# Kernel tuning notes

Hardware: AMD Instinct MI355X
Metric: run time of the kernel (lower is better)

Reference implementation:

```python
import jax, jax.numpy as jnp
import numpy as np

LEVELS = [(128, 128), (64, 64), (32, 32), (16, 16)]  # (H_l, W_l) per feature level
N_TOTAL = sum(h * w for h, w in LEVELS)  # 21760
B, D, H, P, L = 2, 256, 8, 4, 4
HD = D // H
FFN_DIM = 1024


def setup_inputs() -> dict:
    key = jax.random.key(0)
    ks = jax.random.split(key, 12)
    s = 0.02  # weight init scale
    return {
        'embed': jax.random.normal(ks[0], (B, N_TOTAL, D), jnp.float32),
        'pos': jax.random.normal(ks[1], (B, N_TOTAL, D), jnp.float32),
        'ref_points': jax.random.uniform(ks[2], (B, N_TOTAL, L, 2), jnp.float32),
        'ln1_w': jnp.ones((D,), jnp.float32), 'ln1_b': jnp.zeros((D,), jnp.float32),
        'ln2_w': jnp.ones((D,), jnp.float32), 'ln2_b': jnp.zeros((D,), jnp.float32),
        'Wv': jax.random.normal(ks[3], (D, D), jnp.float32) * s, 'bv': jnp.zeros((D,), jnp.float32),
        'Woff': jax.random.normal(ks[4], (D, H * L * P * 2), jnp.float32) * s, 'boff': jnp.zeros((H * L * P * 2,), jnp.float32),
        'Wattn': jax.random.normal(ks[5], (D, H * L * P), jnp.float32) * s, 'battn': jnp.zeros((H * L * P,), jnp.float32),
        'Wo': jax.random.normal(ks[6], (D, D), jnp.float32) * s, 'bo': jnp.zeros((D,), jnp.float32),
        'W1': jax.random.normal(ks[7], (D, FFN_DIM), jnp.float32) * s, 'b1': jnp.zeros((FFN_DIM,), jnp.float32),
        'W2': jax.random.normal(ks[8], (FFN_DIM, D), jnp.float32) * s, 'b2': jnp.zeros((D,), jnp.float32),
        'dimensions': jnp.array(LEVELS, jnp.int32),
    }


def _layer_norm(x, w, b):
    m = jnp.mean(x, axis=-1, keepdims=True)
    v = jnp.mean(jnp.square(x - m), axis=-1, keepdims=True)
    return (x - m) * jax.lax.rsqrt(v + 1e-5) * w + b


def _msda(q, ref, v, dims, Wv, bv, Woff, boff, Wattn, battn, Wo, bo):
    # q, v: (B, N, D); ref: (B, N, L, 2) normalized (x, y)
    Bq, N, _ = q.shape
    value = (v @ Wv + bv).reshape(Bq, N, H, HD)
    off = (q @ Woff + boff).reshape(Bq, N, H, L, P, 2)
    aw = jax.nn.softmax((q @ Wattn + battn).reshape(Bq, N, H, L * P), axis=-1)
    aw = aw.reshape(Bq, N, H, L, P)
    # offset normalizer is [W_l, H_l]
    norm = jnp.stack([dims[:, 1], dims[:, 0]], axis=-1).astype(q.dtype)  # (L, 2)
    loc = ref[:, :, None, :, None, :] + off / norm[None, None, None, :, None, :]  # (B,N,H,L,P,2)

    out = jnp.zeros((Bq, N, H, HD), q.dtype)
    start = 0
    for l, (Hl, Wl) in enumerate(LEVELS):
        S = Hl * Wl
        vl = value[:, start:start + S].transpose(0, 2, 1, 3)  # (B, H, S, hd)
        start += S
        # grid_sample semantics: align_corners=False, zero padding
        x = loc[:, :, :, l, :, 0] * Wl - 0.5  # (B, N, H, P)
        y = loc[:, :, :, l, :, 1] * Hl - 0.5
        x0 = jnp.floor(x); y0 = jnp.floor(y)
        wx = x - x0; wy = y - y0
        x0i = x0.astype(jnp.int32); y0i = y0.astype(jnp.int32)
        samp = jnp.zeros(x.shape + (HD,), q.dtype)
        for dy, dx, w in ((0, 0, (1 - wx) * (1 - wy)), (0, 1, wx * (1 - wy)),
                          (1, 0, (1 - wx) * wy), (1, 1, wx * wy)):
            xi = x0i + dx; yi = y0i + dy
            valid = (xi >= 0) & (xi < Wl) & (yi >= 0) & (yi < Hl)
            idx = jnp.clip(yi, 0, Hl - 1) * Wl + jnp.clip(xi, 0, Wl - 1)  # (B, N, H, P)
            idx_t = idx.transpose(0, 2, 1, 3).reshape(Bq, H, N * P)
            g = jnp.take_along_axis(vl, idx_t[..., None], axis=2)  # (B, H, N*P, hd)
            g = g.reshape(Bq, H, N, P, HD).transpose(0, 2, 1, 3, 4)  # (B, N, H, P, hd)
            samp = samp + (w * valid)[..., None] * g
        out = out + jnp.sum(samp * aw[:, :, :, l, :, None], axis=3)
    return out.reshape(Bq, N, D) @ Wo + bo


def reference(embed, pos, ref_points, ln1_w, ln1_b, ln2_w, ln2_b, Wv, bv, Woff, boff,
              Wattn, battn, Wo, bo, W1, b1, W2, b2, dimensions):
    v = _layer_norm(embed, ln1_w, ln1_b)
    q = v + pos
    embed = embed + _msda(q, ref_points, v, dimensions, Wv, bv, Woff, boff, Wattn, battn, Wo, bo)
    f = _layer_norm(embed, ln2_w, ln2_b)
    embed = embed + jax.nn.relu(f @ W1 + b1) @ W2 + b2
    return embed
```

## Files before the change

### kernel.cpp

```cpp
#include <hip/hip_runtime.h>
#include <cstdint>
#include <cstddef>

#define N_TOTAL 21760
#define BATCH   2
#define M_TOT   (BATCH * N_TOTAL)
#define DMODEL  256
#define NHEAD   8
#define HDIM    32
#define FFN     1024

typedef __bf16 b16x8 __attribute__((ext_vector_type(8)));
typedef float  f32x4 __attribute__((ext_vector_type(4)));

typedef const __attribute__((address_space(1))) void g_void;
typedef __attribute__((address_space(3))) void lds_void;

__device__ __forceinline__ unsigned short f2b(float f) {
  union { float f; unsigned u; } v; v.f = f;
  unsigned r = v.u + 0x7FFF + ((v.u >> 16) & 1);
  return (unsigned short)(r >> 16);
}
__device__ __forceinline__ float b2f(unsigned short u) {
  union { unsigned u; float f; } v; v.u = (unsigned)u << 16;
  return v.f;
}

__global__ void wconv_all(const float* __restrict__ Wv, const float* __restrict__ Woff,
                          const float* __restrict__ Wattn, const float* __restrict__ Wo,
                          const float* __restrict__ W1, const float* __restrict__ W2,
                          unsigned short* __restrict__ dstbase) {
  int idx = blockIdx.x * 256 + threadIdx.x;
  const float* src; int K, N, off;
  if (idx < 65536)       { src = Wv;    K = 256;  N = 256;  off = 0;      }
  else if (idx < 131072) { src = Woff;  K = 256;  N = 256;  off = 65536;  idx -= 65536; }
  else if (idx < 163840) { src = Wattn; K = 256;  N = 128;  off = 131072; idx -= 131072; }
  else if (idx < 229376) { src = Wo;    K = 256;  N = 256;  off = 163840; idx -= 163840; }
  else if (idx < 491520) { src = W1;    K = 256;  N = 1024; off = 229376; idx -= 229376; }
  else if (idx < 753664) { src = W2;    K = 1024; N = 256;  off = 491520; idx -= 491520; }
  else return;
  int k = idx / N, n = idx - k * N;
  dstbase[off + (size_t)n * K + k] = f2b(src[idx]);
}

__global__ void ln1_kernel(const float* __restrict__ x, const float* __restrict__ pos,
                           const float* __restrict__ w, const float* __restrict__ b,
                           unsigned short* __restrict__ vb, unsigned short* __restrict__ qb) {
  int t = threadIdx.x;
  int tkn = blockIdx.x * 4 + (t >> 6);
  int lane = t & 63;
  size_t base = (size_t)tkn * DMODEL + lane * 4;
  float4 xv = *(const float4*)&x[base];
  float s1 = xv.x + xv.y + xv.z + xv.w;
  float s2 = xv.x * xv.x + xv.y * xv.y + xv.z * xv.z + xv.w * xv.w;
  #pragma unroll
  for (int off = 32; off; off >>= 1) {
    s1 += __shfl_down(s1, off);
    s2 += __shfl_down(s2, off);
  }
  s1 = __shfl(s1, 0); s2 = __shfl(s2, 0);
  float m   = s1 * (1.0f / DMODEL);
  float var = s2 * (1.0f / DMODEL) - m * m;
  float rs  = rsqrtf(var + 1e-5f);
  float4 wv = *(const float4*)&w[lane * 4];
  float4 bv = *(const float4*)&b[lane * 4];
  float4 pv = *(const float4*)&pos[base];
  float o0 = (xv.x - m) * rs * wv.x + bv.x;
  float o1 = (xv.y - m) * rs * wv.y + bv.y;
  float o2 = (xv.z - m) * rs * wv.z + bv.z;
  float o3 = (xv.w - m) * rs * wv.w + bv.w;
  ushort4 vo = {f2b(o0), f2b(o1), f2b(o2), f2b(o3)};
  ushort4 qo = {f2b(o0 + pv.x), f2b(o1 + pv.y), f2b(o2 + pv.z), f2b(o3 + pv.w)};
  *(ushort4*)&vb[base] = vo;
  *(ushort4*)&qb[base] = qo;
}

__global__ void ln2_kernel(const unsigned short* __restrict__ x, const float* __restrict__ w,
                           const float* __restrict__ b, unsigned short* __restrict__ yb) {
  int t = threadIdx.x;
  int tkn = blockIdx.x * 4 + (t >> 6);
  int lane = t & 63;
  size_t base = (size_t)tkn * DMODEL + lane * 4;
  ushort4 xu = *(const ushort4*)&x[base];
  float x0 = b2f(xu.x), x1 = b2f(xu.y), x2 = b2f(xu.z), x3 = b2f(xu.w);
  float s1 = x0 + x1 + x2 + x3;
  float s2 = x0 * x0 + x1 * x1 + x2 * x2 + x3 * x3;
  #pragma unroll
  for (int off = 32; off; off >>= 1) {
    s1 += __shfl_down(s1, off);
    s2 += __shfl_down(s2, off);
  }
  s1 = __shfl(s1, 0); s2 = __shfl(s2, 0);
  float m   = s1 * (1.0f / DMODEL);
  float var = s2 * (1.0f / DMODEL) - m * m;
  float rs  = rsqrtf(var + 1e-5f);
  float4 wv = *(const float4*)&w[lane * 4];
  float4 bv = *(const float4*)&b[lane * 4];
  ushort4 vo = {f2b((x0 - m) * rs * wv.x + bv.x), f2b((x1 - m) * rs * wv.y + bv.y),
                f2b((x2 - m) * rs * wv.z + bv.z), f2b((x3 - m) * rs * wv.w + bv.w)};
  *(ushort4*)&yb[base] = vo;
}

__device__ __forceinline__ void gemm_core(
    const unsigned short* __restrict__ A, const unsigned short* __restrict__ Bt,
    const float* __restrict__ bias,
    const float* __restrict__ addf, const unsigned short* __restrict__ addb,
    float* __restrict__ Cf, unsigned short* __restrict__ Cb,
    int K, int N, int relu, int row0, int col0,
    unsigned short* As, unsigned short* Bs) {
  int t  = threadIdx.x;
  int w  = t >> 6;
  int l  = t & 63;
  int wm = w >> 1, wn = w & 1;
  int lr = l & 15;
  int kq = l >> 4;

  f32x4 acc[4][4];
  #pragma unroll
  for (int i = 0; i < 4; ++i)
    #pragma unroll
    for (int j = 0; j < 4; ++j) acc[i][j] = (f32x4){0.f, 0.f, 0.f, 0.f};

  int srow = (l >> 3);
  int sseg = (l & 7) * 8;

  for (int k0 = 0; k0 < K; k0 += 64) {
    #pragma unroll
    for (int i = 0; i < 4; ++i) {
      int c = w * 4 + i;
      const unsigned short* ga = A  + (size_t)(row0 + c * 8 + srow) * K + k0 + sseg;
      const unsigned short* gb = Bt + (size_t)(col0 + c * 8 + srow) * K + k0 + sseg;
      __builtin_amdgcn_global_load_lds((g_void*)ga, (lds_void*)(As + c * 512), 16, 0, 0);
      __builtin_amdgcn_global_load_lds((g_void*)gb, (lds_void*)(Bs + c * 512), 16, 0, 0);
    }
    __syncthreads();
    #pragma unroll
    for (int kk = 0; kk < 2; ++kk) {
      b16x8 aF[4], bF[4];
      #pragma unroll
      for (int i = 0; i < 4; ++i)
        aF[i] = *(const b16x8*)&As[(wm * 64 + i * 16 + lr) * 64 + kk * 32 + kq * 8];
      #pragma unroll
      for (int j = 0; j < 4; ++j)
        bF[j] = *(const b16x8*)&Bs[(wn * 64 + j * 16 + lr) * 64 + kk * 32 + kq * 8];
      #pragma unroll
      for (int i = 0; i < 4; ++i)
        #pragma unroll
        for (int j = 0; j < 4; ++j)
          acc[i][j] = __builtin_amdgcn_mfma_f32_16x16x32_bf16(aF[i], bF[j], acc[i][j], 0, 0, 0);
    }
    __syncthreads();
  }

  #pragma unroll
  for (int j = 0; j < 4; ++j) {
    int colg = col0 + wn * 64 + j * 16 + lr;
    float bcol = bias[colg];
    #pragma unroll
    for (int i = 0; i < 4; ++i) {
      int r0g = row0 + wm * 64 + i * 16 + kq * 4;
      #pragma unroll
      for (int r = 0; r < 4; ++r) {
        int rowg = r0g + r;
        float o = acc[i][j][r] + bcol;
        if (relu) o = fmaxf(o, 0.0f);
        if (addf) o += addf[(size_t)rowg * N + colg];
        if (addb) o += b2f(addb[(size_t)rowg * N + colg]);
        if (Cf) Cf[(size_t)rowg * N + colg] = o;
        if (Cb) Cb[(size_t)rowg * N + colg] = f2b(o);
      }
    }
  }
}

__global__ __launch_bounds__(256, 3)
void gemm_bf16(const unsigned short* __restrict__ A,
               const unsigned short* __restrict__ Bt,
               const float* __restrict__ bias,
               const float* __restrict__ addf, const unsigned short* __restrict__ addb,
               float* __restrict__ Cf, unsigned short* __restrict__ Cb,
               int K, int N, int relu) {
  __shared__ unsigned short As[128 * 64];
  __shared__ unsigned short Bs[128 * 64];
  gemm_core(A, Bt, bias, addf, addb, Cf, Cb, K, N, relu,
            blockIdx.x * 128, blockIdx.y * 128, As, Bs);
}

__global__ __launch_bounds__(256, 3)
void gemm_proj(const unsigned short* __restrict__ vb,
               const unsigned short* __restrict__ qb,
               const unsigned short* __restrict__ Wvt,
               const unsigned short* __restrict__ Wofft,
               const unsigned short* __restrict__ Wattnt,
               const float* __restrict__ bv, const float* __restrict__ boff,
               const float* __restrict__ battn,
               unsigned short* __restrict__ valb,
               unsigned short* __restrict__ offb,
               unsigned short* __restrict__ awb) {
  __shared__ unsigned short As[128 * 64];
  __shared__ unsigned short Bs[128 * 64];
  int y = blockIdx.y;
  const unsigned short* A; const unsigned short* Bt; const float* bias;
  unsigned short* C; int col0, N;
  if (y < 2)      { A = vb; Bt = Wvt;    bias = bv;    C = valb; col0 = y * 128;       N = 256; }
  else if (y < 4) { A = qb; Bt = Wofft;  bias = boff;  C = offb; col0 = (y - 2) * 128; N = 256; }
  else            { A = qb; Bt = Wattnt; bias = battn; C = awb;  col0 = 0;             N = 128; }
  gemm_core(A, Bt, bias, nullptr, nullptr, nullptr, C, 256, N, 0,
            blockIdx.x * 128, col0, As, Bs);
}

__global__ void msda_kernel(const unsigned short* __restrict__ value,
                            const unsigned short* __restrict__ offb,
                            const unsigned short* __restrict__ awb,
                            const float* __restrict__ ref,
                            unsigned short* __restrict__ outb) {
  __shared__ int2 P[544];
  int tkn = blockIdx.x;
  int t   = threadIdx.x;
  int b   = (tkn >= N_TOTAL) ? 1 : 0;

  if (t < 128) {
    int h = t >> 4, s = t & 15, lev = s >> 2, p = s & 3;
    float lg = b2f(awb[(size_t)tkn * 128 + h * 16 + s]);
    float mx = lg;
    #pragma unroll
    for (int m = 1; m < 16; m <<= 1) mx = fmaxf(mx, __shfl_xor(mx, m, 16));
    float e = __expf(lg - mx);
    float sum = e;
    #pragma unroll
    for (int m = 1; m < 16; m <<= 1) sum += __shfl_xor(sum, m, 16);
    float aw = e / sum;

    const int HL[4] = {128, 64, 32, 16};
    const int ST[4] = {0, 16384, 20480, 21504};
    int Wl = HL[lev];
    float rx = ref[(size_t)tkn * 8 + lev * 2 + 0];
    float ry = ref[(size_t)tkn * 8 + lev * 2 + 1];
    float ox = b2f(offb[(size_t)tkn * 256 + h * 32 + lev * 8 + p * 2 + 0]);
    float oy = b2f(offb[(size_t)tkn * 256 + h * 32 + lev * 8 + p * 2 + 1]);
    float x = rx * (float)Wl + ox - 0.5f;
    float y = ry * (float)Wl + oy - 0.5f;
    float x0f = floorf(x), y0f = floorf(y);
    float wx = x - x0f, wy = y - y0f;
    int x0 = (int)x0f, y0 = (int)y0f;
    float wt[4] = {(1.f - wx) * (1.f - wy), wx * (1.f - wy),
                   (1.f - wx) * wy, wx * wy};
    int base = b * N_TOTAL + ST[lev];
    #pragma unroll
    for (int tp = 0; tp < 4; ++tp) {
      int e4 = s * 4 + tp;
      int idx = h * 68 + (e4 >> 5) * 34 + (e4 & 31);
      int xi = x0 + (tp & 1), yi = y0 + (tp >> 1);
      bool ok = (xi >= 0) & (xi < Wl) & (yi >= 0) & (yi < Wl);
      float wgt = ok ? aw * wt[tp] : 0.f;
      int boff2 = ok ? (((base + yi * Wl + xi) * 256 + h * 32) * 2) : 0;
      P[idx] = (int2){__float_as_int(wgt), boff2};
    }
  }
  __syncthreads();

  int h = t >> 5, g = t & 31, dp = g & 15, half = g >> 4;
  int o = h * 68 + half * 34;
  unsigned doff = dp * 4;
  const char* vbase = (const char*)value;
  float accL = 0.f, accH = 0.f;
  #pragma unroll 8
  for (int j = 0; j < 32; ++j) {
    int2 pr = P[o + j];
    float wgt = __int_as_float(pr.x);
    unsigned v = *(const unsigned*)(vbase + (size_t)((unsigned)pr.y + doff));
    union { unsigned u; float f; } lo, hi;
    lo.u = v << 16;
    hi.u = v & 0xffff0000u;
    accL += wgt * lo.f;
    accH += wgt * hi.f;
  }
  accL += __shfl_xor(accL, 16);
  accH += __shfl_xor(accH, 16);
  if (half == 0) {
    unsigned pk = (unsigned)f2b(accL) | ((unsigned)f2b(accH) << 16);
    *(unsigned*)&outb[(size_t)tkn * 256 + h * 32 + dp * 2] = pk;
  }
}

extern "C" void kernel_launch(void* const* d_in, const int* in_sizes, int n_in,
                              void* d_out, int out_size, void* d_ws, size_t ws_size,
                              hipStream_t stream) {
  const float* embed = (const float*)d_in[0];
  const float* pos   = (const float*)d_in[1];
  const float* refp  = (const float*)d_in[2];
  const float* ln1w  = (const float*)d_in[3];
  const float* ln1b  = (const float*)d_in[4];
  const float* ln2w  = (const float*)d_in[5];
  const float* ln2b  = (const float*)d_in[6];
  const float* Wv    = (const float*)d_in[7];
  const float* bv    = (const float*)d_in[8];
  const float* Woff  = (const float*)d_in[9];
  const float* boff  = (const float*)d_in[10];
  const float* Wattn = (const float*)d_in[11];
  const float* battn = (const float*)d_in[12];
  const float* Wo    = (const float*)d_in[13];
  const float* bo    = (const float*)d_in[14];
  const float* W1    = (const float*)d_in[15];
  const float* b1    = (const float*)d_in[16];
  const float* W2    = (const float*)d_in[17];
  const float* b2    = (const float*)d_in[18];
  float* out = (float*)d_out;
  float* ws  = (float*)d_ws;

  const size_t U = (size_t)M_TOT * DMODEL;
  unsigned short* valb16 = (unsigned short*)ws;
  unsigned short* offb16 = (unsigned short*)(ws + U / 2);
  unsigned short* awb16  = (unsigned short*)(ws + U);
  unsigned short* msdab  = (unsigned short*)(ws + U + U / 4);
  unsigned short* hid16  = (unsigned short*)ws;
  unsigned short* emb2b  = (unsigned short*)(ws + 2 * U);
  unsigned short* vb16   = (unsigned short*)(ws + 3 * U);
  unsigned short* qb16   = (unsigned short*)(ws + 3 * U + U / 2);
  unsigned short* fb16   = (unsigned short*)(ws + 4 * U);
  unsigned short* wbuf   = (unsigned short*)(ws + 4 * U + U / 2);

  unsigned short* Wvt    = wbuf;
  unsigned short* Wofft  = wbuf + 65536;
  unsigned short* Wattnt = wbuf + 131072;
  unsigned short* Wot    = wbuf + 163840;
  unsigned short* W1t    = wbuf + 229376;
  unsigned short* W2t    = wbuf + 491520;

  wconv_all<<<(753664 + 255) / 256, 256, 0, stream>>>(Wv, Woff, Wattn, Wo, W1, W2, wbuf);

  ln1_kernel<<<M_TOT / 4, 256, 0, stream>>>(embed, pos, ln1w, ln1b, vb16, qb16);

  gemm_proj<<<dim3(M_TOT / 128, 5), 256, 0, stream>>>(
      vb16, qb16, Wvt, Wofft, Wattnt, bv, boff, battn, valb16, offb16, awb16);

  msda_kernel<<<M_TOT, 256, 0, stream>>>(valb16, offb16, awb16, refp, msdab);

  gemm_bf16<<<dim3(M_TOT / 128, 2), 256, 0, stream>>>(
      msdab, Wot, bo, embed, nullptr, nullptr, emb2b, 256, 256, 0);

  ln2_kernel<<<M_TOT / 4, 256, 0, stream>>>(emb2b, ln2w, ln2b, fb16);

  gemm_bf16<<<dim3(M_TOT / 128, 8), 256, 0, stream>>>(
      fb16, W1t, b1, nullptr, nullptr, nullptr, hid16, 256, 1024, 1);
  gemm_bf16<<<dim3(M_TOT / 128, 2), 256, 0, stream>>>(
      hid16, W2t, b2, nullptr, emb2b, out, nullptr, 1024, 256, 0);
}
```

Before: 316.0 us.

## Remap workgroup IDs so neighbouring tiles share an XCD's L2 cache

```diff
diff --git a/kernel.cpp b/kernel.cpp
--- a/kernel.cpp
+++ b/kernel.cpp
@@ -24,6 +24,12 @@
 __device__ __forceinline__ float b2f(unsigned short u) {
   union { unsigned u; float f; } v; v.u = (unsigned)u << 16;
   return v.f;
+}
+
+__device__ __forceinline__ int xcd_wgid(int bid, int nwg) {
+  int q = nwg >> 3, r = nwg & 7;
+  int xcd = bid & 7, k = bid >> 3;
+  return (xcd < r ? xcd * (q + 1) : r * (q + 1) + (xcd - r) * q) + k;
 }
 
 __global__ void wconv_all(const float* __restrict__ Wv, const float* __restrict__ Woff,
@@ -179,11 +185,13 @@
                const float* __restrict__ bias,
                const float* __restrict__ addf, const unsigned short* __restrict__ addb,
                float* __restrict__ Cf, unsigned short* __restrict__ Cb,
-               int K, int N, int relu) {
+               int K, int N, int relu, int ncolt) {
   __shared__ unsigned short As[128 * 64];
   __shared__ unsigned short Bs[128 * 64];
-  gemm_core(A, Bt, bias, addf, addb, Cf, Cb, K, N, relu,
-            blockIdx.x * 128, blockIdx.y * 128, As, Bs);
+  int wgid = xcd_wgid(blockIdx.x, gridDim.x);
+  int row0 = (wgid / ncolt) * 128;
+  int col0 = (wgid % ncolt) * 128;
+  gemm_core(A, Bt, bias, addf, addb, Cf, Cb, K, N, relu, row0, col0, As, Bs);
 }
 
 __global__ __launch_bounds__(256, 3)
@@ -199,14 +207,15 @@
                unsigned short* __restrict__ awb) {
   __shared__ unsigned short As[128 * 64];
   __shared__ unsigned short Bs[128 * 64];
-  int y = blockIdx.y;
+  int wgid = xcd_wgid(blockIdx.x, gridDim.x);
+  int y = wgid % 5;
+  int row0 = (wgid / 5) * 128;
   const unsigned short* A; const unsigned short* Bt; const float* bias;
   unsigned short* C; int col0, N;
   if (y < 2)      { A = vb; Bt = Wvt;    bias = bv;    C = valb; col0 = y * 128;       N = 256; }
   else if (y < 4) { A = qb; Bt = Wofft;  bias = boff;  C = offb; col0 = (y - 2) * 128; N = 256; }
   else            { A = qb; Bt = Wattnt; bias = battn; C = awb;  col0 = 0;             N = 128; }
-  gemm_core(A, Bt, bias, nullptr, nullptr, nullptr, C, 256, N, 0,
-            blockIdx.x * 128, col0, As, Bs);
+  gemm_core(A, Bt, bias, nullptr, nullptr, nullptr, C, 256, N, 0, row0, col0, As, Bs);
 }
 
 __global__ void msda_kernel(const unsigned short* __restrict__ value,
@@ -215,7 +224,8 @@
                             const float* __restrict__ ref,
                             unsigned short* __restrict__ outb) {
   __shared__ int2 P[544];
-  int tkn = blockIdx.x;
+  int bid = blockIdx.x;
+  int tkn = (bid & 7) * (M_TOT / 8) + (bid >> 3);
   int t   = threadIdx.x;
   int b   = (tkn >= N_TOTAL) ? 1 : 0;
 
@@ -331,18 +341,18 @@
 
   ln1_kernel<<<M_TOT / 4, 256, 0, stream>>>(embed, pos, ln1w, ln1b, vb16, qb16);
 
-  gemm_proj<<<dim3(M_TOT / 128, 5), 256, 0, stream>>>(
+  gemm_proj<<<(M_TOT / 128) * 5, 256, 0, stream>>>(
       vb16, qb16, Wvt, Wofft, Wattnt, bv, boff, battn, valb16, offb16, awb16);
 
   msda_kernel<<<M_TOT, 256, 0, stream>>>(valb16, offb16, awb16, refp, msdab);
 
-  gemm_bf16<<<dim3(M_TOT / 128, 2), 256, 0, stream>>>(
-      msdab, Wot, bo, embed, nullptr, nullptr, emb2b, 256, 256, 0);
+  gemm_bf16<<<(M_TOT / 128) * 2, 256, 0, stream>>>(
+      msdab, Wot, bo, embed, nullptr, nullptr, emb2b, 256, 256, 0, 2);
 
   ln2_kernel<<<M_TOT / 4, 256, 0, stream>>>(emb2b, ln2w, ln2b, fb16);
 
-  gemm_bf16<<<dim3(M_TOT / 128, 8), 256, 0, stream>>>(
-      fb16, W1t, b1, nullptr, nullptr, nullptr, hid16, 256, 1024, 1);
-  gemm_bf16<<<dim3(M_TOT / 128, 2), 256, 0, stream>>>(
-      hid16, W2t, b2, nullptr, emb2b, out, nullptr, 1024, 256, 0);
-}
+  gemm_bf16<<<(M_TOT / 128) * 8, 256, 0, stream>>>(
+      fb16, W1t, b1, nullptr, nullptr, nullptr, hid16, 256, 1024, 1, 8);
+  gemm_bf16<<<(M_TOT / 128) * 2, 256, 0, stream>>>(
+      hid16, W2t, b2, nullptr, emb2b, out, nullptr, 1024, 256, 0, 2);
+}
```

Result: faster. 304.2 us (-3.7%).
